# Performance work log

Measured on AMD Instinct MI355X. Metric: run time of the kernel, lower is better.

## Reference

```python
import jax, jax.numpy as jnp
import numpy as np

S, B, H = 2048, 32, 1024

def setup_inputs() -> dict:
    key = jax.random.key(0)
    ks = jax.random.split(key, 5)
    hidden = jax.random.normal(ks[0], (B, H), dtype=jnp.float32)
    encoder_outputs = jax.random.normal(ks[1], (S, B, H), dtype=jnp.float32)
    source_lengths = jax.random.randint(ks[2], (B,), 1, S + 1, dtype=jnp.int32)
    attn_w = jax.random.normal(ks[3], (H, 2 * H), dtype=jnp.float32) / np.sqrt(2 * H)
    attn_b = jnp.zeros((H,), dtype=jnp.float32)
    v = jax.random.uniform(ks[4], (H,), dtype=jnp.float32)
    return {"hidden": hidden, "encoder_outputs": encoder_outputs,
            "source_lengths": source_lengths, "attn_w": attn_w,
            "attn_b": attn_b, "v": v}

def reference(hidden, encoder_outputs, source_lengths, attn_w, attn_b, v):
    s, b, h = encoder_outputs.shape
    # Broadcast decoder hidden over source positions: (S,B,H)
    hid = jnp.broadcast_to(hidden[None, :, :], (s, b, h))
    cat = jnp.concatenate([hid, encoder_outputs], axis=2)          # (S,B,2H)
    energy = jnp.tanh(jnp.einsum('sbk,hk->sbh', cat, attn_w) + attn_b)  # (S,B,H)
    scores = jnp.einsum('sbh,h->bs', energy, v)                     # (B,S)
    mask = jnp.arange(s)[None, :] < source_lengths[:, None]         # (B,S)
    scores = jnp.where(mask, scores, jnp.float32(-1e10))
    attention_weights = jax.nn.softmax(scores, axis=1)              # (B,S)
    context = jnp.einsum('bs,sbh->bh', attention_weights, encoder_outputs)
    return context, attention_weights
```

## Files before the change

### kernel.cpp

```cpp
#include <hip/hip_runtime.h>

#define S_DIM 2048
#define B_DIM 32
#define H_DIM 1024
#define ROWS  (S_DIM * B_DIM)

typedef __attribute__((ext_vector_type(4))) float    f32x4;
typedef __attribute__((ext_vector_type(8))) _Float16 f16x8;


__device__ __forceinline__ unsigned short f16_bits(float f) {
  union { _Float16 h; unsigned short u; } cv;
  cv.h = (_Float16)f;
  return cv.u;
}

__device__ __forceinline__ float fast_tanh(float x) {
  x = fminf(15.0f, fmaxf(-15.0f, x));
  float z = __expf(-2.0f * x);
  return (1.0f - z) * __builtin_amdgcn_rcpf(1.0f + z);
}

__device__ __forceinline__ void load_lds16(const void* g, void* l) {
  __builtin_amdgcn_global_load_lds(
      (const __attribute__((address_space(1))) unsigned int*)g,
      (__attribute__((address_space(3))) unsigned int*)l, 16, 0, 0);
}

__global__ void convT_kernel(const float* __restrict__ enc,
                             unsigned short* __restrict__ Ep) {
  int step = blockIdx.x, t = blockIdx.y, tid = threadIdx.x;
  const float* src = enc + (size_t)t * 128 * H_DIM + step * 64;
  unsigned short* dst = Ep + (((size_t)t * 16 + step) * 1024) * 8;
#pragma unroll
  for (int c = 0; c < 4; ++c) {
    int q = c * 256 + tid;
    int r = q >> 3, slot = q & 7;
    int sub = slot ^ (r & 7);
    const float* s = src + (size_t)r * H_DIM + sub * 8;
    f32x4 a = *(const f32x4*)s;
    f32x4 b = *(const f32x4*)(s + 4);
    ushort4 lo, hi;
    lo.x = f16_bits(a.x); lo.y = f16_bits(a.y); lo.z = f16_bits(a.z); lo.w = f16_bits(a.w);
    hi.x = f16_bits(b.x); hi.y = f16_bits(b.y); hi.z = f16_bits(b.z); hi.w = f16_bits(b.w);
    *(ushort4*)(dst + q * 8)     = lo;
    *(ushort4*)(dst + q * 8 + 4) = hi;
  }
}

__global__ void prep_kernel(const float* __restrict__ hidden,
                            const float* __restrict__ attn_w,
                            const float* __restrict__ attn_b,
                            float* __restrict__ hp,
                            unsigned short* __restrict__ Bp,
                            float* __restrict__ scores,
                            float* __restrict__ ctx) {
  int bid = blockIdx.x, tid = threadIdx.x;
  if (bid < 64) {
    int hl = tid >> 4;
    int kp = tid & 15;
    int h  = bid * 16 + hl;
    const f32x4* wrow = (const f32x4*)(attn_w + (size_t)h * (2 * H_DIM)) + kp * 16;
    f32x4 w[16];
#pragma unroll
    for (int j = 0; j < 16; ++j) w[j] = wrow[j];
    float bias = attn_b[h];
    for (int b = 0; b < B_DIM; ++b) {
      const f32x4* xrow = (const f32x4*)(hidden + (size_t)b * H_DIM) + kp * 16;
      float s = 0.f;
#pragma unroll
      for (int j = 0; j < 16; ++j) {
        f32x4 x = xrow[j];
        s = fmaf(w[j].x, x.x, s); s = fmaf(w[j].y, x.y, s);
        s = fmaf(w[j].z, x.z, s); s = fmaf(w[j].w, x.w, s);
      }
      s += __shfl_xor(s, 1); s += __shfl_xor(s, 2);
      s += __shfl_xor(s, 4); s += __shfl_xor(s, 8);
      if (kp == 0) hp[(size_t)b * H_DIM + h] = s + bias;
    }
  } else if (bid < 576) {
    int id = (bid - 64) * 256 + tid;
    int slot = id & 7;
    int n    = (id >> 3) & 127;
    int step = (id >> 10) & 15;
    int g    = id >> 14;
    int sub  = slot ^ (n & 7);
    int h    = g * 128 + n;
    const float* src = attn_w + (size_t)h * (2 * H_DIM) + H_DIM + step * 64 + sub * 8;
    f32x4 a = *(const f32x4*)src;
    f32x4 b = *(const f32x4*)(src + 4);
    ushort4 lo, hi;
    lo.x = f16_bits(a.x); lo.y = f16_bits(a.y); lo.z = f16_bits(a.z); lo.w = f16_bits(a.w);
    hi.x = f16_bits(b.x); hi.y = f16_bits(b.y); hi.z = f16_bits(b.z); hi.w = f16_bits(b.w);
    *(ushort4*)(Bp + (size_t)id * 8)     = lo;
    *(ushort4*)(Bp + (size_t)id * 8 + 4) = hi;
  } else if (bid < 640) {
    int idx = (bid - 576) * 256 + tid;
    *(f32x4*)(scores + (size_t)idx * 4) = (f32x4){0.f, 0.f, 0.f, 0.f};
  } else {
    int idx = (bid - 640) * 256 + tid;
    *(f32x4*)(ctx + (size_t)idx * 4) = (f32x4){0.f, 0.f, 0.f, 0.f};
  }
}

__global__ __launch_bounds__(256, 4)
void gemm_scores_kernel(const unsigned short* __restrict__ Ep,
                        const unsigned short* __restrict__ Bp,
                        const float* __restrict__ hp,
                        const float* __restrict__ v,
                        float* __restrict__ scores) {
  __shared__ __align__(16) unsigned short As[1024 * 8];
  __shared__ __align__(16) unsigned short Bs[1024 * 8];
  const int tid  = threadIdx.x;
  const int lane = tid & 63;
  const int wid  = tid >> 6;
  const int wm   = wid >> 1;
  const int wn   = wid & 1;
  const int m16  = lane & 15;
  const int quad = lane >> 4;
  const int rx   = m16 & 7;
  const int bid  = blockIdx.x;
  const int xcd  = bid & 7;
  const int slot = bid >> 3;
  const int t    = xcd * 64 + (slot >> 3);
  const int g    = slot & 7;

  f32x4 acc[4][4];
#pragma unroll
  for (int i = 0; i < 4; ++i)
#pragma unroll
    for (int j = 0; j < 4; ++j) acc[i][j] = (f32x4){0.f, 0.f, 0.f, 0.f};

  const unsigned short* aBase = Ep + (size_t)t * 16 * 8192;
  const unsigned short* bBase = Bp + (size_t)g * 16 * 8192;

  for (int step = 0; step < 16; ++step) {
    const unsigned short* aS = aBase + (size_t)step * 8192;
    const unsigned short* bS = bBase + (size_t)step * 8192;
#pragma unroll
    for (int c = 0; c < 4; ++c) {
      int q = c * 256 + tid;
      load_lds16(aS + (size_t)q * 8, As + q * 8);
      load_lds16(bS + (size_t)q * 8, Bs + q * 8);
    }
    __syncthreads();

#pragma unroll
    for (int ko = 0; ko < 2; ++ko) {
      int sl = (ko * 4 + quad) ^ rx;
      f16x8 af[4], bfr[4];
#pragma unroll
      for (int f = 0; f < 4; ++f) {
        int r = wm * 64 + f * 16 + m16;
        af[f] = *(const f16x8*)&As[r * 64 + sl * 8];
      }
#pragma unroll
      for (int f = 0; f < 4; ++f) {
        int n = wn * 64 + f * 16 + m16;
        bfr[f] = *(const f16x8*)&Bs[n * 64 + sl * 8];
      }
#pragma unroll
      for (int mf = 0; mf < 4; ++mf)
#pragma unroll
        for (int nf = 0; nf < 4; ++nf)
          acc[mf][nf] = __builtin_amdgcn_mfma_f32_16x16x32_f16(
              af[mf], bfr[nf], acc[mf][nf], 0, 0, 0);
    }
    __syncthreads();
  }

  const int row0 = t * 128, n0 = g * 128;
#pragma unroll
  for (int mf = 0; mf < 4; ++mf) {
#pragma unroll
    for (int reg = 0; reg < 4; ++reg) {
      int row_g = row0 + wm * 64 + mf * 16 + quad * 4 + reg;
      int b     = row_g & 31;
      int s     = row_g >> 5;
      float psum = 0.f;
#pragma unroll
      for (int nf = 0; nf < 4; ++nf) {
        int col = n0 + wn * 64 + nf * 16 + m16;
        float e = acc[mf][nf][reg] + hp[b * H_DIM + col];
        e = fast_tanh(e);
        psum = fmaf(e, v[col], psum);
      }
      psum += __shfl_xor(psum, 1);
      psum += __shfl_xor(psum, 2);
      psum += __shfl_xor(psum, 4);
      psum += __shfl_xor(psum, 8);
      if (m16 == 0) atomicAdd(&scores[b * S_DIM + s], psum);
    }
  }
}

__global__ void softmax_kernel(const float* __restrict__ scores,
                               const int* __restrict__ lens,
                               float* __restrict__ wout) {
  int b = blockIdx.x, tid = threadIdx.x;
  int len = lens[b];
  float vals[8];
  float m = -3.0e38f;
#pragma unroll
  for (int i = 0; i < 8; ++i) {
    int s = i * 256 + tid;
    float x = scores[b * S_DIM + s];
    vals[i] = (s < len) ? x : -3.0e38f;
    m = fmaxf(m, vals[i]);
  }
#pragma unroll
  for (int off = 32; off > 0; off >>= 1) m = fmaxf(m, __shfl_xor(m, off));
  __shared__ float redm[4], reds[4];
  int wid = tid >> 6, lane = tid & 63;
  if (lane == 0) redm[wid] = m;
  __syncthreads();
  m = fmaxf(fmaxf(redm[0], redm[1]), fmaxf(redm[2], redm[3]));

  float e[8];
  float sum = 0.f;
#pragma unroll
  for (int i = 0; i < 8; ++i) {
    int s = i * 256 + tid;
    e[i] = (s < len) ? __expf(vals[i] - m) : 0.f;
    sum += e[i];
  }
#pragma unroll
  for (int off = 32; off > 0; off >>= 1) sum += __shfl_xor(sum, off);
  if (lane == 0) reds[wid] = sum;
  __syncthreads();
  sum = reds[0] + reds[1] + reds[2] + reds[3];
  float inv = 1.0f / sum;
#pragma unroll
  for (int i = 0; i < 8; ++i)
    wout[b * S_DIM + i * 256 + tid] = e[i] * inv;
}

__global__ void context_kernel(const unsigned short* __restrict__ Ep,
                               const float* __restrict__ wts,
                               const int* __restrict__ lens,
                               float* __restrict__ ctx) {
  int sc = blockIdx.x;
  int b0 = blockIdx.y * 2;
  int tid = threadIdx.x;
  int bb = tid >> 7;
  int c  = tid & 127;
  int b  = b0 + bb;
  int len = lens[b];
  int s0 = sc * 64;
  if (s0 >= len) return;
  int cnt = min(64, len - s0);
  int step = c >> 3, sub = c & 7;
  int slot = sub ^ (b & 7);
  int hb = step * 64 + sub * 8;
  float acc[8] = {0.f, 0.f, 0.f, 0.f, 0.f, 0.f, 0.f, 0.f};
  const float* wrow = wts + (size_t)b * S_DIM + s0;
  for (int i = 0; i < cnt; ++i) {
    int s = s0 + i;
    float w = wrow[i];
    int t = s >> 2;
    int r = (s & 3) * 32 + b;
    size_t chunk = ((size_t)t * 16 + step) * 1024 + r * 8 + slot;
    f16x8 e = *(const f16x8*)(Ep + chunk * 8);
#pragma unroll
    for (int j = 0; j < 8; ++j) acc[j] = fmaf(w, (float)e[j], acc[j]);
  }
  float* dst = ctx + (size_t)b * H_DIM + hb;
#pragma unroll
  for (int j = 0; j < 8; ++j) atomicAdd(dst + j, acc[j]);
}

extern "C" void kernel_launch(void* const* d_in, const int* in_sizes, int n_in,
                              void* d_out, int out_size, void* d_ws, size_t ws_size,
                              hipStream_t stream) {
  const float* hidden = (const float*)d_in[0];
  const float* enc    = (const float*)d_in[1];
  const int*   lens   = (const int*)d_in[2];
  const float* attn_w = (const float*)d_in[3];
  const float* attn_b = (const float*)d_in[4];
  const float* v      = (const float*)d_in[5];

  float* out_ctx = (float*)d_out;
  float* out_w   = (float*)d_out + B_DIM * H_DIM;

  char* p = (char*)d_ws;
  unsigned short* Ep = (unsigned short*)p; p += (size_t)ROWS * H_DIM * 2;
  float* scores = (float*)p;               p += (size_t)B_DIM * S_DIM * 4;
  float* hp     = (float*)p;               p += (size_t)B_DIM * H_DIM * 4;
  unsigned short* Bp = (unsigned short*)p;

  hipLaunchKernelGGL(convT_kernel, dim3(16, ROWS / 128), dim3(256), 0, stream,
                     enc, Ep);
  hipLaunchKernelGGL(prep_kernel, dim3(672), dim3(256), 0, stream,
                     hidden, attn_w, attn_b, hp, Bp, scores, out_ctx);
  hipLaunchKernelGGL(gemm_scores_kernel, dim3(4096), dim3(256), 0, stream,
                     Ep, Bp, hp, v, scores);
  hipLaunchKernelGGL(softmax_kernel, dim3(B_DIM), dim3(256), 0, stream,
                     scores, lens, out_w);
  hipLaunchKernelGGL(context_kernel, dim3(S_DIM / 64, B_DIM / 2), dim3(256),
                     0, stream, Ep, out_w, lens, out_ctx);
}
```

Before: 663.8 us.

## Fuse fp32-to-fp16 encoder conversion into GEMM tile load, drop convT pass

Removes the separate pass that converted the encoder outputs to a swizzled fp16 copy. The GEMM now reads fp32 encoder rows directly, converts them in registers with packed round-toward-zero conversion and stores them into LDS. The context kernel reads fp32 encoder data directly, with one batch per block and 128 positions per block. This avoids writing and re-reading a large intermediate buffer, but the GEMM A-tile load becomes a synchronous register path instead of an async global-to-LDS copy, and the context kernel reads twice as many bytes per element.

```diff
diff --git a/kernel.cpp b/kernel.cpp
--- a/kernel.cpp
+++ b/kernel.cpp
@@ -7,7 +7,7 @@
 
 typedef __attribute__((ext_vector_type(4))) float    f32x4;
 typedef __attribute__((ext_vector_type(8))) _Float16 f16x8;
-
+typedef __attribute__((ext_vector_type(2))) __fp16   h16x2;
 
 __device__ __forceinline__ unsigned short f16_bits(float f) {
   union { _Float16 h; unsigned short u; } cv;
@@ -25,27 +25,6 @@
   __builtin_amdgcn_global_load_lds(
       (const __attribute__((address_space(1))) unsigned int*)g,
       (__attribute__((address_space(3))) unsigned int*)l, 16, 0, 0);
-}
-
-__global__ void convT_kernel(const float* __restrict__ enc,
-                             unsigned short* __restrict__ Ep) {
-  int step = blockIdx.x, t = blockIdx.y, tid = threadIdx.x;
-  const float* src = enc + (size_t)t * 128 * H_DIM + step * 64;
-  unsigned short* dst = Ep + (((size_t)t * 16 + step) * 1024) * 8;
-#pragma unroll
-  for (int c = 0; c < 4; ++c) {
-    int q = c * 256 + tid;
-    int r = q >> 3, slot = q & 7;
-    int sub = slot ^ (r & 7);
-    const float* s = src + (size_t)r * H_DIM + sub * 8;
-    f32x4 a = *(const f32x4*)s;
-    f32x4 b = *(const f32x4*)(s + 4);
-    ushort4 lo, hi;
-    lo.x = f16_bits(a.x); lo.y = f16_bits(a.y); lo.z = f16_bits(a.z); lo.w = f16_bits(a.w);
-    hi.x = f16_bits(b.x); hi.y = f16_bits(b.y); hi.z = f16_bits(b.z); hi.w = f16_bits(b.w);
-    *(ushort4*)(dst + q * 8)     = lo;
-    *(ushort4*)(dst + q * 8 + 4) = hi;
-  }
 }
 
 __global__ void prep_kernel(const float* __restrict__ hidden,
@@ -104,7 +83,7 @@
 }
 
 __global__ __launch_bounds__(256, 4)
-void gemm_scores_kernel(const unsigned short* __restrict__ Ep,
+void gemm_scores_kernel(const float* __restrict__ enc,
                         const unsigned short* __restrict__ Bp,
                         const float* __restrict__ hp,
                         const float* __restrict__ v,
@@ -131,17 +110,36 @@
 #pragma unroll
     for (int j = 0; j < 4; ++j) acc[i][j] = (f32x4){0.f, 0.f, 0.f, 0.f};
 
-  const unsigned short* aBase = Ep + (size_t)t * 16 * 8192;
+  const float* aBase = enc + (size_t)t * 128 * H_DIM;
   const unsigned short* bBase = Bp + (size_t)g * 16 * 8192;
 
+  int aR[4], aSub[4];
+#pragma unroll
+  for (int c = 0; c < 4; ++c) {
+    int q = c * 256 + tid;
+    aR[c] = q >> 3;
+    aSub[c] = (q & 7) ^ (aR[c] & 7);
+  }
+
   for (int step = 0; step < 16; ++step) {
-    const unsigned short* aS = aBase + (size_t)step * 8192;
     const unsigned short* bS = bBase + (size_t)step * 8192;
 #pragma unroll
     for (int c = 0; c < 4; ++c) {
       int q = c * 256 + tid;
-      load_lds16(aS + (size_t)q * 8, As + q * 8);
       load_lds16(bS + (size_t)q * 8, Bs + q * 8);
+    }
+#pragma unroll
+    for (int c = 0; c < 4; ++c) {
+      int q = c * 256 + tid;
+      const float* s = aBase + (size_t)aR[c] * H_DIM + step * 64 + aSub[c] * 8;
+      f32x4 a = *(const f32x4*)s;
+      f32x4 b = *(const f32x4*)(s + 4);
+      union { f16x8 v8; h16x2 h2[4]; } pk;
+      pk.h2[0] = __builtin_amdgcn_cvt_pkrtz(a.x, a.y);
+      pk.h2[1] = __builtin_amdgcn_cvt_pkrtz(a.z, a.w);
+      pk.h2[2] = __builtin_amdgcn_cvt_pkrtz(b.x, b.y);
+      pk.h2[3] = __builtin_amdgcn_cvt_pkrtz(b.z, b.w);
+      *(f16x8*)(As + q * 8) = pk.v8;
     }
     __syncthreads();
 
@@ -235,38 +233,33 @@
     wout[b * S_DIM + i * 256 + tid] = e[i] * inv;
 }
 
-__global__ void context_kernel(const unsigned short* __restrict__ Ep,
+__global__ void context_kernel(const float* __restrict__ enc,
                                const float* __restrict__ wts,
                                const int* __restrict__ lens,
                                float* __restrict__ ctx) {
   int sc = blockIdx.x;
-  int b0 = blockIdx.y * 2;
+  int b  = blockIdx.y;
+  int len = lens[b];
+  int s0 = sc * 128;
+  if (s0 >= len) return;
+  int cnt = min(128, len - s0);
   int tid = threadIdx.x;
-  int bb = tid >> 7;
-  int c  = tid & 127;
-  int b  = b0 + bb;
-  int len = lens[b];
-  int s0 = sc * 64;
-  if (s0 >= len) return;
-  int cnt = min(64, len - s0);
-  int step = c >> 3, sub = c & 7;
-  int slot = sub ^ (b & 7);
-  int hb = step * 64 + sub * 8;
-  float acc[8] = {0.f, 0.f, 0.f, 0.f, 0.f, 0.f, 0.f, 0.f};
+  f32x4 acc = (f32x4){0.f, 0.f, 0.f, 0.f};
   const float* wrow = wts + (size_t)b * S_DIM + s0;
+#pragma unroll 4
   for (int i = 0; i < cnt; ++i) {
-    int s = s0 + i;
     float w = wrow[i];
-    int t = s >> 2;
-    int r = (s & 3) * 32 + b;
-    size_t chunk = ((size_t)t * 16 + step) * 1024 + r * 8 + slot;
-    f16x8 e = *(const f16x8*)(Ep + chunk * 8);
-#pragma unroll
-    for (int j = 0; j < 8; ++j) acc[j] = fmaf(w, (float)e[j], acc[j]);
-  }
-  float* dst = ctx + (size_t)b * H_DIM + hb;
-#pragma unroll
-  for (int j = 0; j < 8; ++j) atomicAdd(dst + j, acc[j]);
+    f32x4 e = *(const f32x4*)(enc + ((size_t)(s0 + i) * B_DIM + b) * H_DIM + tid * 4);
+    acc.x = fmaf(w, e.x, acc.x);
+    acc.y = fmaf(w, e.y, acc.y);
+    acc.z = fmaf(w, e.z, acc.z);
+    acc.w = fmaf(w, e.w, acc.w);
+  }
+  float* dst = ctx + (size_t)b * H_DIM + tid * 4;
+  atomicAdd(dst + 0, acc.x);
+  atomicAdd(dst + 1, acc.y);
+  atomicAdd(dst + 2, acc.z);
+  atomicAdd(dst + 3, acc.w);
 }
 
 extern "C" void kernel_launch(void* const* d_in, const int* in_sizes, int n_in,
@@ -283,19 +276,16 @@
   float* out_w   = (float*)d_out + B_DIM * H_DIM;
 
   char* p = (char*)d_ws;
-  unsigned short* Ep = (unsigned short*)p; p += (size_t)ROWS * H_DIM * 2;
   float* scores = (float*)p;               p += (size_t)B_DIM * S_DIM * 4;
   float* hp     = (float*)p;               p += (size_t)B_DIM * H_DIM * 4;
   unsigned short* Bp = (unsigned short*)p;
 
-  hipLaunchKernelGGL(convT_kernel, dim3(16, ROWS / 128), dim3(256), 0, stream,
-                     enc, Ep);
   hipLaunchKernelGGL(prep_kernel, dim3(672), dim3(256), 0, stream,
                      hidden, attn_w, attn_b, hp, Bp, scores, out_ctx);
   hipLaunchKernelGGL(gemm_scores_kernel, dim3(4096), dim3(256), 0, stream,
-                     Ep, Bp, hp, v, scores);
+                     enc, Bp, hp, v, scores);
   hipLaunchKernelGGL(softmax_kernel, dim3(B_DIM), dim3(256), 0, stream,
                      scores, lens, out_w);
-  hipLaunchKernelGGL(context_kernel, dim3(S_DIM / 64, B_DIM / 2), dim3(256),
-                     0, stream, Ep, out_w, lens, out_ctx);
-}
+  hipLaunchKernelGGL(context_kernel, dim3(16, B_DIM), dim3(256), 0, stream,
+                     enc, out_w, lens, out_ctx);
+}
```

Measured after the change: 604.8 us. -8.9%, faster.
